# Kernel tuning notes

Measured on AMD Instinct MI355X. Metric: run time of the kernel, lower is better.

Reference implementation:

```python
import jax, jax.numpy as jnp
import numpy as np

EMB = 64
N_LEFT = 50000
N_RIGHT = 50000
N_EDGES = 1000000
EPS = 1e-5


def _block(x, w1, b1, w2, b2):
    # Linear -> BatchNorm1d(batch stats, no affine) -> (Dropout=id, eval) -> Linear -> ReLU
    h = x @ w1 + b1
    mu = h.mean(axis=0)
    var = h.var(axis=0)  # biased, matches torch BN normalization
    h = (h - mu) / jnp.sqrt(var + EPS)
    return jax.nn.relu(h @ w2 + b2)


def _lin_init(key, fan_in, fan_out):
    k1, k2 = jax.random.split(key)
    bound = 1.0 / np.sqrt(fan_in)
    w = jax.random.uniform(k1, (fan_in, fan_out), minval=-bound, maxval=bound, dtype=jnp.float32)
    b = jax.random.uniform(k2, (fan_out,), minval=-bound, maxval=bound, dtype=jnp.float32)
    return w, b


def setup_inputs() -> dict:
    key = jax.random.key(0)
    ks = jax.random.split(key, 16)
    inp = {}
    inp['left_features'] = jax.random.normal(ks[0], (N_LEFT, EMB), dtype=jnp.float32)
    inp['right_features'] = jax.random.normal(ks[1], (N_RIGHT, EMB), dtype=jnp.float32)
    inp['edge_features'] = jax.random.normal(ks[2], (N_EDGES, EMB), dtype=jnp.float32)
    src = jax.random.randint(ks[3], (N_EDGES,), 0, N_LEFT, dtype=jnp.int32)
    dst = jax.random.randint(ks[4], (N_EDGES,), 0, N_RIGHT, dtype=jnp.int32)
    inp['edge_index'] = jnp.stack([src, dst], axis=0)
    # feature_module_right (applied to both i and j, as in the original message())
    inp['fmr_w1'], inp['fmr_b1'] = _lin_init(ks[5], EMB, EMB)
    inp['fmr_w2'], inp['fmr_b2'] = _lin_init(ks[6], EMB, EMB)
    # feature_module_edge
    inp['fme_w1'], inp['fme_b1'] = _lin_init(ks[7], EMB, EMB)
    inp['fme_w2'], inp['fme_b2'] = _lin_init(ks[8], EMB, EMB)
    # feature_module_final (3*emb -> emb -> emb)
    inp['fmf_w1'], inp['fmf_b1'] = _lin_init(ks[9], 3 * EMB, EMB)
    inp['fmf_w2'], inp['fmf_b2'] = _lin_init(ks[10], EMB, EMB)
    # output_module (2*emb -> emb -> emb)
    inp['out_w1'], inp['out_b1'] = _lin_init(ks[11], 2 * EMB, EMB)
    inp['out_w2'], inp['out_b2'] = _lin_init(ks[12], EMB, EMB)
    return inp


def reference(left_features, right_features, edge_features, edge_index,
              fmr_w1, fmr_b1, fmr_w2, fmr_b2,
              fme_w1, fme_b1, fme_w2, fme_b2,
              fmf_w1, fmf_b1, fmf_w2, fmf_b2,
              out_w1, out_b1, out_w2, out_b2):
    src = edge_index[0]  # index into left (source / j)
    dst = edge_index[1]  # index into right (target / i)

    x_i = right_features[dst]           # [E, emb] gathered targets
    x_j = left_features[src]            # [E, emb] gathered sources

    m_i = _block(x_i, fmr_w1, fmr_b1, fmr_w2, fmr_b2)
    m_e = _block(edge_features, fme_w1, fme_b1, fme_w2, fme_b2)
    m_j = _block(x_j, fmr_w1, fmr_b1, fmr_w2, fmr_b2)  # feature_module_right reused, as in source

    msg = _block(jnp.concatenate([m_i, m_e, m_j], axis=1),
                 fmf_w1, fmf_b1, fmf_w2, fmf_b2)        # [E, emb]

    # mean aggregation over target nodes
    agg = jax.ops.segment_sum(msg, dst, num_segments=N_RIGHT)
    cnt = jax.ops.segment_sum(jnp.ones((msg.shape[0],), msg.dtype), dst, num_segments=N_RIGHT)
    agg = agg / jnp.maximum(cnt, 1.0)[:, None]

    out = _block(jnp.concatenate([agg, right_features], axis=1),
                 out_w1, out_b1, out_w2, out_b2)        # [N_right, emb]
    return out
```

## Files before the change

### kernel.cpp

```cpp
#include <hip/hip_runtime.h>

#define EMB 64
#define BNEPS 1e-5f
#define NSLAB 8
#define NSLABH 32
#define MAXSLOT 128
#define MAXOVF 65536

typedef unsigned short u16;
typedef float f32x4 __attribute__((ext_vector_type(4)));
typedef short bf16x8 __attribute__((ext_vector_type(8)));
typedef short bf16x4 __attribute__((ext_vector_type(4)));

__device__ __forceinline__ float bf2f(u16 u){
  union { unsigned int i; float f; } v; v.i = ((unsigned int)u) << 16; return v.f;
}
__device__ __forceinline__ u16 f2bf(float x){
  union { float f; unsigned int i; } v; v.f = x;
  unsigned int r = v.i + 0x7FFFu + ((v.i >> 16) & 1u);
  return (u16)(r >> 16);
}
__device__ __forceinline__ void atomAddF(float* p, float v){
  __hip_atomic_fetch_add(p, v, __ATOMIC_RELAXED, __HIP_MEMORY_SCOPE_AGENT);
}

__global__ void kzero(float* __restrict__ fz, long nf){
  long i0 = (long)blockIdx.x * blockDim.x + threadIdx.x;
  long st = (long)gridDim.x * blockDim.x;
  for (long i = i0; i < nf; i += st) fz[i] = 0.f;
}

__global__ void kcount(const int* __restrict__ src, const int* __restrict__ dst,
                       int E, int* __restrict__ cs, int* __restrict__ cd,
                       int* __restrict__ sort1, int* __restrict__ ovfCnt,
                       int* __restrict__ ovfList){
  int e = blockIdx.x * blockDim.x + threadIdx.x;
  int st = gridDim.x * blockDim.x;
  for (; e < E; e += st){
    atomicAdd(&cs[src[e]], 1);
    int d = dst[e];
    int i = atomicAdd(&cd[d], 1);
    if (sort1){
      if (i < MAXSLOT){
        sort1[(size_t)d * MAXSLOT + i] = e;
      } else {
        int oi = atomicAdd(ovfCnt, 1);
        if (oi < MAXOVF) ovfList[oi] = e;
      }
    }
  }
}

__global__ __launch_bounds__(1024) void ktiles(const int* __restrict__ cd, int NR,
                       int* __restrict__ tcnt, int* __restrict__ tlist){
  __shared__ int wsum[16];
  __shared__ int wbase[16];
  __shared__ int bbase;
  int tid = threadIdx.x, lane = tid & 63, w = tid >> 6;
  int d = blockIdx.x * 1024 + tid;
  int nt = 0, c = 0;
  if (d < NR){
    c = cd[d];
    if (c > 0){
      nt = (c + 15) >> 4;
      if (nt > (MAXSLOT / 16)) nt = MAXSLOT / 16;
    }
  }
  int inc = nt;
  #pragma unroll
  for (int m = 1; m < 64; m <<= 1){
    int v = __shfl_up(inc, m);
    if (lane >= m) inc += v;
  }
  if (lane == 63) wsum[w] = inc;
  __syncthreads();
  if (tid == 0){
    int acc = 0;
    #pragma unroll
    for (int k = 0; k < 16; k++){ wbase[k] = acc; acc += wsum[k]; }
    bbase = acc ? atomicAdd(tcnt, acc) : 0;
  }
  __syncthreads();
  int my = bbase + wbase[w] + inc - nt;
  for (int t = 0; t < nt; t++){
    int vc = c - t * 16; if (vc > 16) vc = 16;
    tlist[my + t] = (vc << 20) | (d << 3) | t;
  }
}

__global__ __launch_bounds__(256) void kgram(const float* __restrict__ X,
    const int* __restrict__ cnt, int N,
    float* __restrict__ mupart, float* __restrict__ Spart){
  __shared__ float xs[16][EMB];
  __shared__ float cs[16];
  int t = threadIdx.x;
  int a = t >> 2, bb = (t & 3) << 4;
  int row = t >> 4, k0 = (t & 15) << 2;
  float g[16];
  #pragma unroll
  for (int i = 0; i < 16; i++) g[i] = 0.f;
  float mup = 0.f;
  int base0 = blockIdx.x * 16, stride = gridDim.x * 16;
  f32x4 xreg = {0.f,0.f,0.f,0.f};
  float creg = 0.f;
  {
    int n = base0 + row;
    if (n < N) xreg = *(const f32x4*)(X + (size_t)n * EMB + k0);
    if (t < 16){
      int n2 = base0 + t;
      creg = (n2 < N) ? (float)cnt[n2] : 0.f;
    }
  }
  for (int n0 = base0; n0 < N; n0 += stride){
    *(f32x4*)&xs[row][k0] = xreg;
    if (t < 16) cs[t] = creg;
    __syncthreads();
    int n1 = n0 + stride;
    if (n1 < N){
      int n = n1 + row;
      xreg = (n < N) ? *(const f32x4*)(X + (size_t)n * EMB + k0) : (f32x4){0.f,0.f,0.f,0.f};
      if (t < 16){
        int n2 = n1 + t;
        creg = (n2 < N) ? (float)cnt[n2] : 0.f;
      }
    }
    #pragma unroll
    for (int rr = 0; rr < 16; rr++){
      float xa = cs[rr] * xs[rr][a];
      const float4* x4 = (const float4*)&xs[rr][bb];
      #pragma unroll
      for (int i4 = 0; i4 < 4; i4++){
        float4 v = x4[i4];
        g[4*i4+0] += xa * v.x; g[4*i4+1] += xa * v.y;
        g[4*i4+2] += xa * v.z; g[4*i4+3] += xa * v.w;
      }
    }
    if (t < EMB){
      #pragma unroll
      for (int rr = 0; rr < 16; rr++) mup += cs[rr] * xs[rr][t];
    }
    __syncthreads();
  }
  float* Sp = Spart + (size_t)blockIdx.x * 4096;
  #pragma unroll
  for (int i4 = 0; i4 < 4; i4++)
    *(f32x4*)&Sp[a * EMB + bb + i4 * 4] = *(f32x4*)&g[i4 * 4];
  if (t < EMB) mupart[(size_t)blockIdx.x * 64 + t] = mup;
}

struct GredArgs { const float *Sp, *mp; int nb; float *So, *mo; };
__global__ __launch_bounds__(256) void kgreduce3(GredArgs g0, GredArgs g1, GredArgs g2){
  int job = blockIdx.x >> 4, sub = blockIdx.x & 15;
  GredArgs G = (job == 0) ? g0 : (job == 1) ? g1 : g2;
  int e = sub * 256 + threadIdx.x;
  float s0 = 0.f, s1 = 0.f, s2 = 0.f, s3 = 0.f;
  int b = 0;
  for (; b + 3 < G.nb; b += 4){
    s0 += G.Sp[(size_t)(b    ) * 4096 + e];
    s1 += G.Sp[(size_t)(b + 1) * 4096 + e];
    s2 += G.Sp[(size_t)(b + 2) * 4096 + e];
    s3 += G.Sp[(size_t)(b + 3) * 4096 + e];
  }
  for (; b < G.nb; b++) s0 += G.Sp[(size_t)b * 4096 + e];
  G.So[e] = (s0 + s1) + (s2 + s3);
  if (sub == 0 && threadIdx.x < 64){
    float m0 = 0.f, m1 = 0.f, m2 = 0.f, m3 = 0.f;
    int c = 0;
    for (; c + 3 < G.nb; c += 4){
      m0 += G.mp[(size_t)(c    ) * 64 + threadIdx.x];
      m1 += G.mp[(size_t)(c + 1) * 64 + threadIdx.x];
      m2 += G.mp[(size_t)(c + 2) * 64 + threadIdx.x];
      m3 += G.mp[(size_t)(c + 3) * 64 + threadIdx.x];
    }
    for (; c < G.nb; c++) m0 += G.mp[(size_t)c * 64 + threadIdx.x];
    G.mo[threadIdx.x] = (m0 + m1) + (m2 + m3);
  }
}

__global__ __launch_bounds__(256) void kprepm(const float* __restrict__ XE, int N,
    float* __restrict__ mupart, float* __restrict__ Spart, u16* __restrict__ XEb){
  __shared__ __align__(16) u16 XT[64 * 72];
  int t = threadIdx.x, l = t & 63, wv = t >> 6, g = l >> 4, e16 = l & 15;
  f32x4 C[4];
  #pragma unroll
  for (int mb = 0; mb < 4; mb++) C[mb] = (f32x4){0.f,0.f,0.f,0.f};
  float ms[4] = {0.f, 0.f, 0.f, 0.f};
  int ntiles = N >> 6;
  int T = blockIdx.x;
  f32x4 vr0 = {0,0,0,0}, vr1 = {0,0,0,0}, vr2 = {0,0,0,0}, vr3 = {0,0,0,0};
  if (T < ntiles){
    #pragma unroll
    for (int i = 0; i < 4; i++){
      int c = t + i * 256;
      int row = c >> 4, k0 = (c & 15) << 2;
      f32x4 v = *(const f32x4*)(XE + ((size_t)T * 64 + row) * EMB + k0);
      if (i == 0) vr0 = v; else if (i == 1) vr1 = v; else if (i == 2) vr2 = v; else vr3 = v;
    }
  }
  for (; T < ntiles; T += gridDim.x){
    #pragma unroll
    for (int i = 0; i < 4; i++){
      int c = t + i * 256;
      int row = c >> 4, k0 = (c & 15) << 2;
      f32x4 v = (i == 0) ? vr0 : (i == 1) ? vr1 : (i == 2) ? vr2 : vr3;
      u16 w4[4];
      #pragma unroll
      for (int q = 0; q < 4; q++){
        ms[q] += v[q];
        w4[q] = f2bf(v[q]);
        XT[(k0 + q) * 72 + row] = w4[q];
      }
      if (XEb) *(bf16x4*)(XEb + ((size_t)T * 64 + row) * EMB + k0) = *(bf16x4*)w4;
    }
    __syncthreads();
    int T2 = T + gridDim.x;
    if (T2 < ntiles){
      #pragma unroll
      for (int i = 0; i < 4; i++){
        int c = t + i * 256;
        int row = c >> 4, k0 = (c & 15) << 2;
        f32x4 v = *(const f32x4*)(XE + ((size_t)T2 * 64 + row) * EMB + k0);
        if (i == 0) vr0 = v; else if (i == 1) vr1 = v; else if (i == 2) vr2 = v; else vr3 = v;
      }
    }
    #pragma unroll
    for (int kf = 0; kf < 2; kf++){
      bf16x8 fr[4];
      #pragma unroll
      for (int mb = 0; mb < 4; mb++)
        fr[mb] = *(const bf16x8*)&XT[(mb*16 + e16) * 72 + kf*32 + g*8];
      bf16x8 bfr = *(const bf16x8*)&XT[(wv*16 + e16) * 72 + kf*32 + g*8];
      #pragma unroll
      for (int mb = 0; mb < 4; mb++)
        C[mb] = __builtin_amdgcn_mfma_f32_16x16x32_bf16(fr[mb], bfr, C[mb], 0, 0, 0);
    }
    __syncthreads();
  }
  float* Sp = Spart + (size_t)blockIdx.x * 4096;
  #pragma unroll
  for (int mb = 0; mb < 4; mb++)
    #pragma unroll
    for (int r = 0; r < 4; r++)
      Sp[(mb*16 + g*4 + r) * EMB + wv*16 + e16] = C[mb][r];
  __syncthreads();
  float* red = (float*)XT;
  #pragma unroll
  for (int q = 0; q < 4; q++){
    float x = ms[q];
    x += __shfl_xor(x, 16); x += __shfl_xor(x, 32);
    if (l < 16) red[(wv*16 + l)*4 + q] = x;
  }
  __syncthreads();
  if (t < 64){
    int k = t >> 2, q = t & 3;
    float s = red[(k)*4+q] + red[(16+k)*4+q] + red[(32+k)*4+q] + red[(48+k)*4+q];
    mupart[(size_t)blockIdx.x * 64 + k*4 + q] = s;
  }
}

struct EffwArgs {
  const float *mu, *S, *w1, *b1, *w2, *b2;
  float *We, *be;
};
__global__ __launch_bounds__(256) void keffw3(EffwArgs a0, EffwArgs a1, EffwArgs a2,
    float invN, u16* __restrict__ fragA1, u16* __restrict__ fragA2,
    const float* __restrict__ fA2src){
  EffwArgs A = (blockIdx.x == 0) ? a0 : (blockIdx.x == 1) ? a1 : a2;
  const float *musum = A.mu, *S = A.S, *w1 = A.w1, *b1 = A.b1, *w2 = A.w2, *b2 = A.b2;
  float *Weff = A.We, *beff = A.be;
  __shared__ float mu[EMB];
  __shared__ float C[EMB][EMB];
  __shared__ float W1p[EMB][EMB + 1];
  __shared__ float c1[EMB];
  __shared__ float istd[EMB];
  __shared__ float red[256];
  int t = threadIdx.x;
  if (t < EMB) mu[t] = musum[t] * invN;
  __syncthreads();
  for (int e = t; e < EMB * EMB; e += 256){
    int k = e >> 6, l = e & 63;
    C[k][l] = S[e] * invN - mu[k] * mu[l];
  }
  __syncthreads();
  {
    int j = t & 63, kg = t >> 6;
    float part = 0.f;
    for (int k = kg * 16; k < kg * 16 + 16; k++){
      float inner = 0.f;
      for (int l = 0; l < EMB; l++) inner += C[k][l] * w1[l * EMB + j];
      part += w1[k * EMB + j] * inner;
    }
    red[t] = part;
  }
  __syncthreads();
  if (t < EMB){
    float var = red[t] + red[t + 64] + red[t + 128] + red[t + 192];
    float is = 1.0f / sqrtf(var + BNEPS);
    istd[t] = is;
    float muh = 0.f;
    for (int k = 0; k < EMB; k++) muh += mu[k] * w1[k * EMB + t];
    muh += b1[t];
    c1[t] = (b1[t] - muh) * is;
  }
  __syncthreads();
  for (int e = t; e < EMB * EMB; e += 256){
    int k = e >> 6, j = e & 63;
    W1p[k][j] = w1[e] * istd[j];
  }
  __syncthreads();
  {
    int k = t >> 2, j2b = (t & 3) << 4;
    float acc[16];
    #pragma unroll
    for (int i = 0; i < 16; i++) acc[i] = 0.f;
    for (int j = 0; j < EMB; j++){
      float wp = W1p[k][j];
      const float* w2r = &w2[j * EMB + j2b];
      #pragma unroll
      for (int i = 0; i < 16; i++) acc[i] += wp * w2r[i];
    }
    #pragma unroll
    for (int i = 0; i < 16; i++){
      Weff[k * EMB + j2b + i] = acc[i];
      C[k][j2b + i] = acc[i];
    }
  }
  if (t < EMB){
    float acc = b2[t];
    for (int j = 0; j < EMB; j++) acc += c1[j] * w2[j * EMB + t];
    beff[t] = acc;
  }
  __syncthreads();
  if (blockIdx.x == 2){
    for (int ent = t; ent < 512; ent += 256){
      int mb = ent >> 7, kf = (ent >> 6) & 1, l = ent & 63;
      int g = l >> 4, e16 = l & 15;
      u16 out[8];
      #pragma unroll
      for (int i = 0; i < 8; i++)
        out[i] = f2bf(C[kf*32 + g*8 + i][mb*16 + e16]);
      *(bf16x8*)(fragA1 + ent * 8) = *(bf16x8*)out;
    }
  } else if (blockIdx.x == 1){
    for (int ent = t; ent < 512; ent += 256){
      int mb = ent >> 7, kf = (ent >> 6) & 1, l = ent & 63;
      int g = l >> 4, e16 = l & 15;
      u16 out[8];
      #pragma unroll
      for (int i = 0; i < 8; i++){
        int row = (kf + 2*(i>>2))*16 + g*4 + (i&3);
        out[i] = f2bf(fA2src[row * EMB + mb*16 + e16]);
      }
      *(bf16x8*)(fragA2 + ent * 8) = *(bf16x8*)out;
    }
  }
}

__global__ __launch_bounds__(256) void knodeMP(const float* __restrict__ X,
    const float* __restrict__ Weff, const float* __restrict__ beff,
    const float* __restrict__ Wslice, int N, u16* __restrict__ P){
  __shared__ float xs[4][EMB];
  __shared__ float ms[4][EMB];
  __shared__ float be[EMB];
  int t = threadIdx.x, r = t >> 6, j = t & 63;
  float wA[EMB], wB[EMB];
  #pragma unroll
  for (int k = 0; k < EMB; k++){ wA[k] = Weff[k * EMB + j]; wB[k] = Wslice[k * EMB + j]; }
  if (t < EMB) be[t] = beff[t];
  __syncthreads();
  for (int n0 = blockIdx.x * 4; n0 < N; n0 += gridDim.x * 4){
    int n = n0 + r; bool ok = n < N;
    xs[r][j] = ok ? X[(size_t)n * EMB + j] : 0.f;
    __syncthreads();
    float a0 = be[j], a1 = 0.f, a2 = 0.f, a3 = 0.f;
    const float4* x4 = (const float4*)xs[r];
    #pragma unroll
    for (int kb = 0; kb < 16; kb++){
      float4 v = x4[kb];
      a0 += v.x * wA[4*kb]; a1 += v.y * wA[4*kb+1];
      a2 += v.z * wA[4*kb+2]; a3 += v.w * wA[4*kb+3];
    }
    ms[r][j] = fmaxf((a0 + a1) + (a2 + a3), 0.f);
    __syncthreads();
    float p0 = 0.f, p1 = 0.f, p2 = 0.f, p3 = 0.f;
    const float4* m4 = (const float4*)ms[r];
    #pragma unroll
    for (int kb = 0; kb < 16; kb++){
      float4 v = m4[kb];
      p0 += v.x * wB[4*kb]; p1 += v.y * wB[4*kb+1];
      p2 += v.z * wB[4*kb+2]; p3 += v.w * wB[4*kb+3];
    }
    if (ok) P[(size_t)n * EMB + j] = f2bf((p0 + p1) + (p2 + p3));
    __syncthreads();
  }
}

__global__ __launch_bounds__(256) void kpass1m(const float* __restrict__ XE,
    const u16* __restrict__ XEb,
    const int* __restrict__ srcv, const int* __restrict__ dstv,
    const u16* __restrict__ fragA1, const u16* __restrict__ fragA2,
    const float* __restrict__ beff_e, const float* __restrict__ bf1,
    const u16* __restrict__ Pib, const u16* __restrict__ Pjb, int ntiles,
    u16* __restrict__ hbf, float* __restrict__ hsum, float* __restrict__ hsq){
  __shared__ float cs[256];
  int t = threadIdx.x, l = t & 63, wv = t >> 6, g = l >> 4, e16 = l & 15;
  cs[t] = 0.f;
  bf16x8 a1w[4][2], a2w[4][2];
  #pragma unroll
  for (int mb = 0; mb < 4; mb++)
    #pragma unroll
    for (int kf = 0; kf < 2; kf++){
      a1w[mb][kf] = *(const bf16x8*)(fragA1 + ((size_t)((mb*2+kf)*64 + l)) * 8);
      a2w[mb][kf] = *(const bf16x8*)(fragA2 + ((size_t)((mb*2+kf)*64 + l)) * 8);
    }
  f32x4 b1v[4], b2v[4];
  #pragma unroll
  for (int mb = 0; mb < 4; mb++)
    #pragma unroll
    for (int r = 0; r < 4; r++){
      b1v[mb][r] = beff_e[mb*16 + g*4 + r];
      b2v[mb][r] = bf1[mb*16 + g*4 + r];
    }
  f32x4 ps[4], pq[4];
  #pragma unroll
  for (int mb = 0; mb < 4; mb++){ ps[mb] = (f32x4){0,0,0,0}; pq[mb] = (f32x4){0,0,0,0}; }

  int gw = blockIdx.x * 4 + wv, nw = gridDim.x * 4;
  int d_n = 0, s_n = 0;
  if (gw < ntiles){ d_n = dstv[gw*16 + e16]; s_n = srcv[gw*16 + e16]; }
  for (int T = gw; T < ntiles; T += nw){
    int d = d_n, s = s_n;
    bf16x8 xf0, xf1;
    if (XEb){
      const u16* xr = XEb + (size_t)(T*16 + e16) * EMB;
      xf0 = *(const bf16x8*)(xr + g*8);
      xf1 = *(const bf16x8*)(xr + 32 + g*8);
    } else {
      const float* xr = XE + (size_t)(T*16 + e16) * EMB;
      f32x4 x0 = *(const f32x4*)(xr + g*8);
      f32x4 x1 = *(const f32x4*)(xr + g*8 + 4);
      f32x4 x2 = *(const f32x4*)(xr + 32 + g*8);
      f32x4 x3 = *(const f32x4*)(xr + 36 + g*8);
      #pragma unroll
      for (int q = 0; q < 4; q++){
        xf0[q]   = (short)f2bf(x0[q]); xf0[4+q] = (short)f2bf(x1[q]);
        xf1[q]   = (short)f2bf(x2[q]); xf1[4+q] = (short)f2bf(x3[q]);
      }
    }
    const u16* pib = Pib + (size_t)d * EMB;
    const u16* pjb = Pjb + (size_t)s * EMB;
    bf16x4 piv[4], pjv[4];
    #pragma unroll
    for (int mb = 0; mb < 4; mb++){
      piv[mb] = *(const bf16x4*)(pib + mb*16 + g*4);
      pjv[mb] = *(const bf16x4*)(pjb + mb*16 + g*4);
    }
    int T2 = T + nw;
    if (T2 < ntiles){ d_n = dstv[T2*16 + e16]; s_n = srcv[T2*16 + e16]; }
    f32x4 C2[4];
    #pragma unroll
    for (int mb = 0; mb < 4; mb++)
      #pragma unroll
      for (int r = 0; r < 4; r++)
        C2[mb][r] = b2v[mb][r] + bf2f((u16)piv[mb][r]) + bf2f((u16)pjv[mb][r]);
    f32x4 C1[4];
    #pragma unroll
    for (int mb = 0; mb < 4; mb++) C1[mb] = b1v[mb];
    #pragma unroll
    for (int mb = 0; mb < 4; mb++){
      C1[mb] = __builtin_amdgcn_mfma_f32_16x16x32_bf16(a1w[mb][0], xf0, C1[mb], 0, 0, 0);
      C1[mb] = __builtin_amdgcn_mfma_f32_16x16x32_bf16(a1w[mb][1], xf1, C1[mb], 0, 0, 0);
    }
    bf16x8 mfr0, mfr1;
    #pragma unroll
    for (int q = 0; q < 4; q++){
      mfr0[q]   = (short)f2bf(fmaxf(C1[0][q], 0.f));
      mfr0[4+q] = (short)f2bf(fmaxf(C1[2][q], 0.f));
      mfr1[q]   = (short)f2bf(fmaxf(C1[1][q], 0.f));
      mfr1[4+q] = (short)f2bf(fmaxf(C1[3][q], 0.f));
    }
    #pragma unroll
    for (int mb = 0; mb < 4; mb++){
      C2[mb] = __builtin_amdgcn_mfma_f32_16x16x32_bf16(a2w[mb][0], mfr0, C2[mb], 0, 0, 0);
      C2[mb] = __builtin_amdgcn_mfma_f32_16x16x32_bf16(a2w[mb][1], mfr1, C2[mb], 0, 0, 0);
    }
    #pragma unroll
    for (int mb = 0; mb < 4; mb++){ ps[mb] += C2[mb]; pq[mb] += C2[mb] * C2[mb]; }
    u16* hr = hbf + (size_t)(T*16 + e16) * EMB;
    #pragma unroll
    for (int mb = 0; mb < 4; mb++){
      u16 hv[4];
      #pragma unroll
      for (int q = 0; q < 4; q++) hv[q] = f2bf(C2[mb][q]);
      *(bf16x4*)(hr + mb*16 + g*4) = *(bf16x4*)hv;
    }
  }
  __syncthreads();
  #pragma unroll
  for (int mb = 0; mb < 4; mb++)
    #pragma unroll
    for (int r = 0; r < 4; r++){
      float v = ps[mb][r], u = pq[mb][r];
      #pragma unroll
      for (int m = 1; m < 16; m <<= 1){ v += __shfl_xor(v, m); u += __shfl_xor(u, m); }
      if (e16 == 0){
        int col = mb*16 + g*4 + r;
        atomicAdd(&cs[col], v);
        atomicAdd(&cs[128 + col], u);
      }
    }
  __syncthreads();
  int slab = blockIdx.x & (NSLABH - 1);
  if (t < 64) atomAddF(&hsum[slab * 64 + t], cs[t]);
  else if (t < 128) atomAddF(&hsq[slab * 64 + t - 64], cs[128 + t - 64]);
}

__global__ __launch_bounds__(256) void kbnfold(const float* __restrict__ hsum,
    const float* __restrict__ hsq, int nslab, float invN, const float* __restrict__ w2,
    const float* __restrict__ b2, float* __restrict__ W2p, float* __restrict__ b2p,
    u16* __restrict__ F){
  __shared__ float mu[EMB], istd[EMB];
  int t = threadIdx.x;
  if (t < EMB){
    float m = 0.f, q = 0.f;
    for (int s = 0; s < nslab; s++){ m += hsum[s * 64 + t]; q += hsq[s * 64 + t]; }
    m *= invN;
    float var = q * invN - m * m;
    mu[t] = m; istd[t] = 1.0f / sqrtf(var + BNEPS);
  }
  __syncthreads();
  for (int e = t; e < EMB * EMB; e += 256){
    int k = e >> 6;
    W2p[e] = istd[k] * w2[e];
  }
  if (t < EMB){
    float acc = b2[t];
    for (int k = 0; k < EMB; k++) acc -= mu[k] * istd[k] * w2[k * EMB + t];
    b2p[t] = acc;
  }
  if (F){
    for (int ent = t; ent < 512; ent += 256){
      int mb = ent >> 7, kf = (ent >> 6) & 1, l = ent & 63;
      int g = (l >> 4), e16 = l & 15;
      u16 out[8];
      #pragma unroll
      for (int i = 0; i < 8; i++){
        int row = kf*32 + g*8 + i;
        out[i] = f2bf(istd[row] * w2[row * EMB + mb*16 + e16]);
      }
      *(bf16x8*)(F + ent * 8) = *(bf16x8*)out;
    }
  }
}

__global__ __launch_bounds__(256) void kpass2s(const u16* __restrict__ hb,
    const int* __restrict__ sort1, const int* __restrict__ tcnt,
    const int* __restrict__ tlist, const u16* __restrict__ fragW2,
    const float* __restrict__ b2p, float* __restrict__ agg){
  int t = threadIdx.x, l = t & 63, wv = t >> 6, g = l >> 4, e16 = l & 15;
  bf16x8 w2f[4][2];
  #pragma unroll
  for (int nb = 0; nb < 4; nb++)
    #pragma unroll
    for (int kf = 0; kf < 2; kf++)
      w2f[nb][kf] = *(const bf16x8*)(fragW2 + ((size_t)((nb*2+kf)*64 + l)) * 8);
  float bv[4];
  #pragma unroll
  for (int nb = 0; nb < 4; nb++) bv[nb] = b2p[nb*16 + e16];

  int tc = *tcnt;
  int gw = blockIdx.x * 4 + wv, nw = gridDim.x * 4;
  if (gw >= tc) return;
  int w_n = tlist[gw];
  int se_n = sort1[(size_t)((w_n >> 3) & 0x1FFFF) * MAXSLOT + (w_n & 7) * 16 + e16];
  for (int m = gw; m < tc; m += nw){
    int w = w_n, se = se_n;
    int m2 = m + nw;
    if (m2 < tc) w_n = tlist[m2];
    int d = (w >> 3) & 0x1FFFF, vc = w >> 20;
    int eid = (e16 < vc) ? se : 0;
    const u16* hr = hb + (size_t)eid * EMB;
    bf16x8 a0 = *(const bf16x8*)(hr + g*8);
    bf16x8 a1 = *(const bf16x8*)(hr + 32 + g*8);
    if (m2 < tc)
      se_n = sort1[(size_t)((w_n >> 3) & 0x1FFFF) * MAXSLOT + (w_n & 7) * 16 + e16];
    f32x4 C[4];
    #pragma unroll
    for (int nb = 0; nb < 4; nb++) C[nb] = (f32x4){0.f,0.f,0.f,0.f};
    #pragma unroll
    for (int nb = 0; nb < 4; nb++){
      C[nb] = __builtin_amdgcn_mfma_f32_16x16x32_bf16(a0, w2f[nb][0], C[nb], 0, 0, 0);
      C[nb] = __builtin_amdgcn_mfma_f32_16x16x32_bf16(a1, w2f[nb][1], C[nb], 0, 0, 0);
    }
    int r0 = g * 4;
    #pragma unroll
    for (int nb = 0; nb < 4; nb++){
      float s = 0.f;
      if (r0 + 0 < vc) s += fmaxf(C[nb][0] + bv[nb], 0.f);
      if (r0 + 1 < vc) s += fmaxf(C[nb][1] + bv[nb], 0.f);
      if (r0 + 2 < vc) s += fmaxf(C[nb][2] + bv[nb], 0.f);
      if (r0 + 3 < vc) s += fmaxf(C[nb][3] + bv[nb], 0.f);
      s += __shfl_xor(s, 16);
      s += __shfl_xor(s, 32);
      if (g == 0) atomAddF(&agg[(size_t)d * EMB + nb*16 + e16], s);
    }
  }
}

__global__ __launch_bounds__(256) void kpass2d(const u16* __restrict__ hb,
    const int* __restrict__ dstv, const u16* __restrict__ fragW2,
    const float* __restrict__ b2p, int ntiles, float* __restrict__ agg){
  int t = threadIdx.x, l = t & 63, wv = t >> 6, g = l >> 4, e16 = l & 15;
  bf16x8 w2f[4][2];
  #pragma unroll
  for (int nb = 0; nb < 4; nb++)
    #pragma unroll
    for (int kf = 0; kf < 2; kf++)
      w2f[nb][kf] = *(const bf16x8*)(fragW2 + ((size_t)((nb*2+kf)*64 + l)) * 8);
  float bv[4];
  #pragma unroll
  for (int nb = 0; nb < 4; nb++) bv[nb] = b2p[nb*16 + e16];
  int gw = blockIdx.x * 4 + wv, nw = gridDim.x * 4;
  for (int T = gw; T < ntiles; T += nw){
    const u16* hr = hb + (size_t)(T*16 + e16) * EMB;
    bf16x8 a0 = *(const bf16x8*)(hr + g*8);
    bf16x8 a1 = *(const bf16x8*)(hr + 32 + g*8);
    int4 dd = *(const int4*)(dstv + T*16 + g*4);
    f32x4 C[4];
    #pragma unroll
    for (int nb = 0; nb < 4; nb++) C[nb] = (f32x4){0.f,0.f,0.f,0.f};
    #pragma unroll
    for (int nb = 0; nb < 4; nb++){
      C[nb] = __builtin_amdgcn_mfma_f32_16x16x32_bf16(a0, w2f[nb][0], C[nb], 0, 0, 0);
      C[nb] = __builtin_amdgcn_mfma_f32_16x16x32_bf16(a1, w2f[nb][1], C[nb], 0, 0, 0);
    }
    int dr[4] = {dd.x, dd.y, dd.z, dd.w};
    #pragma unroll
    for (int r = 0; r < 4; r++){
      float* ap = agg + (size_t)dr[r] * EMB + e16;
      #pragma unroll
      for (int nb = 0; nb < 4; nb++)
        atomAddF(ap + nb*16, fmaxf(C[nb][r] + bv[nb], 0.f));
    }
  }
}

__global__ void kpass2f(const u16* __restrict__ hb, const int* __restrict__ ovfList,
    const int* __restrict__ ovfCnt, const int* __restrict__ dstv,
    const float* __restrict__ W2p, const float* __restrict__ b2p, float* __restrict__ agg){
  int cnt = *ovfCnt;
  if (cnt > MAXOVF) cnt = MAXOVF;
  for (int c = blockIdx.x * blockDim.x + threadIdx.x; c < cnt * 64;
       c += gridDim.x * blockDim.x){
    int e = ovfList[c >> 6], j = c & 63;
    const u16* hr = hb + (size_t)e * EMB;
    float acc = b2p[j];
    for (int k = 0; k < 64; k++) acc += bf2f(hr[k]) * W2p[k * EMB + j];
    atomAddF(&agg[(size_t)dstv[e] * EMB + j], fmaxf(acc, 0.f));
  }
}

__global__ __launch_bounds__(256) void kout1(const float* __restrict__ agg,
    const int* __restrict__ cnt, const float* __restrict__ right,
    const float* __restrict__ ow1, const float* __restrict__ ob1, int N,
    float* __restrict__ h_o, float* __restrict__ osum, float* __restrict__ osq){
  __shared__ float xs[4][2 * EMB];
  __shared__ float bsh[EMB];
  __shared__ float red[256];
  int t = threadIdx.x, r = t >> 6, j = t & 63;
  float wc[2 * EMB];
  #pragma unroll
  for (int k = 0; k < 2 * EMB; k++) wc[k] = ow1[k * EMB + j];
  if (t < EMB) bsh[t] = ob1[t];
  __syncthreads();
  float psum = 0.f, psq = 0.f;
  for (int n0 = blockIdx.x * 4; n0 < N; n0 += gridDim.x * 4){
    int n = n0 + r; bool ok = n < N;
    if (ok){
      float c = fmaxf((float)cnt[n], 1.f);
      xs[r][j] = agg[(size_t)n * EMB + j] / c;
      xs[r][EMB + j] = right[(size_t)n * EMB + j];
    } else { xs[r][j] = 0.f; xs[r][EMB + j] = 0.f; }
    __syncthreads();
    float a0 = bsh[j], a1 = 0.f, a2 = 0.f, a3 = 0.f;
    const float4* x4 = (const float4*)xs[r];
    #pragma unroll
    for (int kb = 0; kb < 32; kb++){
      float4 v = x4[kb];
      a0 += v.x * wc[4*kb]; a1 += v.y * wc[4*kb+1];
      a2 += v.z * wc[4*kb+2]; a3 += v.w * wc[4*kb+3];
    }
    if (ok){
      float h = (a0 + a1) + (a2 + a3);
      h_o[(size_t)n * EMB + j] = h;
      psum += h; psq += h * h;
    }
    __syncthreads();
  }
  int slab = blockIdx.x & (NSLAB - 1);
  red[t] = psum; __syncthreads();
  if (t < EMB) atomAddF(&osum[slab * 64 + t], red[t] + red[t + 64] + red[t + 128] + red[t + 192]);
  __syncthreads();
  red[t] = psq; __syncthreads();
  if (t < EMB) atomAddF(&osq[slab * 64 + t], red[t] + red[t + 64] + red[t + 128] + red[t + 192]);
}

__global__ __launch_bounds__(256) void kout2(const float* __restrict__ h_o,
    const float* __restrict__ W2o, const float* __restrict__ b2o, int N,
    float* __restrict__ out){
  __shared__ float hs[4][EMB];
  __shared__ float bsh[EMB];
  int t = threadIdx.x, r = t >> 6, j = t & 63;
  float wc[EMB];
  #pragma unroll
  for (int k = 0; k < EMB; k++) wc[k] = W2o[k * EMB + j];
  if (t < EMB) bsh[t] = b2o[t];
  __syncthreads();
  for (int n0 = blockIdx.x * 4; n0 < N; n0 += gridDim.x * 4){
    int n = n0 + r; bool ok = n < N;
    hs[r][j] = ok ? h_o[(size_t)n * EMB + j] : 0.f;
    __syncthreads();
    float a0 = bsh[j], a1 = 0.f, a2 = 0.f, a3 = 0.f;
    const float4* h4 = (const float4*)hs[r];
    #pragma unroll
    for (int kb = 0; kb < 16; kb++){
      float4 v = h4[kb];
      a0 += v.x * wc[4*kb]; a1 += v.y * wc[4*kb+1];
      a2 += v.z * wc[4*kb+2]; a3 += v.w * wc[4*kb+3];
    }
    if (ok) out[(size_t)n * EMB + j] = fmaxf((a0 + a1) + (a2 + a3), 0.f);
    __syncthreads();
  }
}

extern "C" void kernel_launch(void* const* d_in, const int* in_sizes, int n_in,
                              void* d_out, int out_size, void* d_ws, size_t ws_size,
                              hipStream_t stream){
  const float* left   = (const float*)d_in[0];
  const float* right  = (const float*)d_in[1];
  const float* edgef  = (const float*)d_in[2];
  const int*   eidx   = (const int*)d_in[3];
  const float* fmr_w1 = (const float*)d_in[4];  const float* fmr_b1 = (const float*)d_in[5];
  const float* fmr_w2 = (const float*)d_in[6];  const float* fmr_b2 = (const float*)d_in[7];
  const float* fme_w1 = (const float*)d_in[8];  const float* fme_b1 = (const float*)d_in[9];
  const float* fme_w2 = (const float*)d_in[10]; const float* fme_b2 = (const float*)d_in[11];
  const float* fmf_w1 = (const float*)d_in[12]; const float* fmf_b1 = (const float*)d_in[13];
  const float* fmf_w2 = (const float*)d_in[14]; const float* fmf_b2 = (const float*)d_in[15];
  const float* ow1    = (const float*)d_in[16]; const float* ob1    = (const float*)d_in[17];
  const float* ow2    = (const float*)d_in[18]; const float* ob2    = (const float*)d_in[19];

  int NL = in_sizes[0] / EMB;
  int NR = in_sizes[1] / EMB;
  int E  = in_sizes[2] / EMB;
  const int* srcv = eidx;
  const int* dstv = eidx + E;

  char* base = (char*)d_ws;
  size_t o = 0;
  u16* hbf = (u16*)(base + o);      o += (size_t)E * EMB * sizeof(u16);
  u16* P_i  = (u16*)(base + o); o += (size_t)NR * EMB * sizeof(u16);
  u16* P_j  = (u16*)(base + o); o += (size_t)NL * EMB * sizeof(u16);
  float* h_o  = (float*)(base + o); o += (size_t)NR * EMB * 4;
  float* Weff_i = (float*)(base + o); o += EMB * EMB * 4;
  float* beff_i = (float*)(base + o); o += EMB * 4;
  float* Weff_j = (float*)(base + o); o += EMB * EMB * 4;
  float* beff_j = (float*)(base + o); o += EMB * 4;
  float* Weff_e = (float*)(base + o); o += EMB * EMB * 4;
  float* beff_e = (float*)(base + o); o += EMB * 4;
  float* W2p  = (float*)(base + o); o += EMB * EMB * 4;
  float* b2p  = (float*)(base + o); o += EMB * 4;
  float* W2o  = (float*)(base + o); o += EMB * EMB * 4;
  float* b2o  = (float*)(base + o); o += EMB * 4;
  u16* fragA1 = (u16*)(base + o); o += 512 * 8 * sizeof(u16);
  u16* fragA2 = (u16*)(base + o); o += 512 * 8 * sizeof(u16);
  u16* fragW2 = (u16*)(base + o); o += 512 * 8 * sizeof(u16);
  int* ovfList = (int*)(base + o); o += MAXOVF * sizeof(int);
  int* tlist   = (int*)(base + o); o += (size_t)NR * (MAXSLOT / 16) * sizeof(int);
  char* zstart = base + o;
  float* agg     = (float*)(base + o); o += (size_t)NR * EMB * 4;
  int* cnt_dst   = (int*)(base + o);   o += (size_t)NR * 4;
  int* cnt_src   = (int*)(base + o);   o += (size_t)NL * 4;
  int* ovfCnt    = (int*)(base + o);   o += 64;
  int* tileCnt   = (int*)(base + o);   o += 64;
  float* musum_i = (float*)(base + o); o += NSLAB * EMB * 4;
  float* S_i     = (float*)(base + o); o += NSLAB * EMB * EMB * 4;
  float* musum_j = (float*)(base + o); o += NSLAB * EMB * 4;
  float* S_j     = (float*)(base + o); o += NSLAB * EMB * EMB * 4;
  float* musum_e = (float*)(base + o); o += NSLAB * EMB * 4;
  float* S_e     = (float*)(base + o); o += NSLAB * EMB * EMB * 4;
  float* hsum    = (float*)(base + o); o += NSLABH * EMB * 4;
  float* hsq     = (float*)(base + o); o += NSLABH * EMB * 4;
  float* osum    = (float*)(base + o); o += NSLAB * EMB * 4;
  float* osq     = (float*)(base + o); o += NSLAB * EMB * 4;
  long zn = (long)(((base + o) - zstart) / 4);
  int* sort1 = nullptr;
  {
    size_t s1b = (size_t)NR * MAXSLOT * sizeof(int);
    if (o + s1b <= ws_size){ sort1 = (int*)(base + o); o += s1b; }
  }
  u16* XEb = nullptr;
  {
    size_t xeb_bytes = (size_t)E * EMB * sizeof(u16);
    if (o + xeb_bytes <= ws_size){ XEb = (u16*)(base + o); o += xeb_bytes; }
  }

  const int NBG = 512;
  const int NBE = 1024;
  float* Spart_i  = (float*)hbf;
  float* Spart_j  = Spart_i + (size_t)NBG * 4096;
  float* Spart_e  = Spart_j + (size_t)NBG * 4096;
  float* mupart_i = Spart_e + (size_t)NBE * 4096;
  float* mupart_j = mupart_i + (size_t)NBG * 64;
  float* mupart_e = mupart_j + (size_t)NBG * 64;

  float invE = 1.0f / (float)E;
  float invNR = 1.0f / (float)NR;
  int ntE = E >> 4;

  kzero<<<1024, 256, 0, stream>>>((float*)zstart, zn);
  kcount<<<512, 256, 0, stream>>>(srcv, dstv, E, cnt_src, cnt_dst, sort1, ovfCnt, ovfList);
  if (sort1) ktiles<<<(NR + 1023) / 1024, 1024, 0, stream>>>(cnt_dst, NR, tileCnt, tlist);
  kprepm<<<NBE, 256, 0, stream>>>(edgef, E, mupart_e, Spart_e, XEb);
  kgram<<<NBG, 256, 0, stream>>>(right, cnt_dst, NR, mupart_i, Spart_i);
  kgram<<<NBG, 256, 0, stream>>>(left,  cnt_src, NL, mupart_j, Spart_j);
  {
    GredArgs g0 = {Spart_i, mupart_i, NBG, S_i, musum_i};
    GredArgs g1 = {Spart_j, mupart_j, NBG, S_j, musum_j};
    GredArgs g2 = {Spart_e, mupart_e, NBE, S_e, musum_e};
    kgreduce3<<<48, 256, 0, stream>>>(g0, g1, g2);
  }
  {
    EffwArgs a0 = {musum_i, S_i, fmr_w1, fmr_b1, fmr_w2, fmr_b2, Weff_i, beff_i};
    EffwArgs a1 = {musum_j, S_j, fmr_w1, fmr_b1, fmr_w2, fmr_b2, Weff_j, beff_j};
    EffwArgs a2 = {musum_e, S_e, fme_w1, fme_b1, fme_w2, fme_b2, Weff_e, beff_e};
    keffw3<<<3, 256, 0, stream>>>(a0, a1, a2, invE, fragA1, fragA2, fmf_w1 + EMB * EMB);
  }
  knodeMP<<<1024, 256, 0, stream>>>(right, Weff_i, beff_i, fmf_w1,                 NR, P_i);
  knodeMP<<<1024, 256, 0, stream>>>(left,  Weff_j, beff_j, fmf_w1 + 2 * EMB * EMB, NL, P_j);
  kpass1m<<<1536, 256, 0, stream>>>(edgef, XEb, srcv, dstv, fragA1, fragA2, beff_e,
                                    fmf_b1, P_i, P_j, ntE, hbf, hsum, hsq);
  kbnfold<<<1, 256, 0, stream>>>(hsum, hsq, NSLABH, invE, fmf_w2, fmf_b2, W2p, b2p, fragW2);
  if (sort1){
    kpass2s<<<2048, 256, 0, stream>>>(hbf, sort1, tileCnt, tlist, fragW2, b2p, agg);
    kpass2f<<<16, 256, 0, stream>>>(hbf, ovfList, ovfCnt, dstv, W2p, b2p, agg);
  } else {
    kpass2d<<<2048, 256, 0, stream>>>(hbf, dstv, fragW2, b2p, ntE, agg);
  }
  kout1<<<1024, 256, 0, stream>>>(agg, cnt_dst, right, ow1, ob1, NR, h_o, osum, osq);
  kbnfold<<<1, 256, 0, stream>>>(osum, osq, NSLAB, invNR, ow2, ob2, W2o, b2o, (u16*)nullptr);
  kout2<<<1024, 256, 0, stream>>>(h_o, W2o, b2o, NR, (float*)d_out);
}
```

Baseline: 730.3 us.

## Permute node projections for contiguous gathers, fold output BN into kout2

knodeMP now writes each projected node row in a permuted order that matches the MFMA accumulator layout. kpass1m can then fetch each lane's 16 values of the gathered P_i/P_j rows with two 16-byte loads per row, where it previously issued four 8-byte loads per row. The final BN fold kernel is removed and its work is done redundantly in every kout2 block, saving one launch at the cost of each block reading ow2 and the stats. kpass1m's grid also grows from 1536 to 2048 blocks.

Result: faster. 710.7 us (-2.7%).

```diff
diff --git a/kernel.cpp b/kernel.cpp
--- a/kernel.cpp
+++ b/kernel.cpp
@@ -363,6 +363,7 @@
   __shared__ float ms[4][EMB];
   __shared__ float be[EMB];
   int t = threadIdx.x, r = t >> 6, j = t & 63;
+  int pos = ((j >> 2) & 3) * 16 + (j >> 4) * 4 + (j & 3);
   float wA[EMB], wB[EMB];
   #pragma unroll
   for (int k = 0; k < EMB; k++){ wA[k] = Weff[k * EMB + j]; wB[k] = Wslice[k * EMB + j]; }
@@ -390,7 +391,7 @@
       p0 += v.x * wB[4*kb]; p1 += v.y * wB[4*kb+1];
       p2 += v.z * wB[4*kb+2]; p3 += v.w * wB[4*kb+3];
     }
-    if (ok) P[(size_t)n * EMB + j] = f2bf((p0 + p1) + (p2 + p3));
+    if (ok) P[(size_t)n * EMB + pos] = f2bf((p0 + p1) + (p2 + p3));
     __syncthreads();
   }
 }
@@ -447,22 +448,23 @@
         xf1[q]   = (short)f2bf(x2[q]); xf1[4+q] = (short)f2bf(x3[q]);
       }
     }
-    const u16* pib = Pib + (size_t)d * EMB;
-    const u16* pjb = Pjb + (size_t)s * EMB;
-    bf16x4 piv[4], pjv[4];
-    #pragma unroll
-    for (int mb = 0; mb < 4; mb++){
-      piv[mb] = *(const bf16x4*)(pib + mb*16 + g*4);
-      pjv[mb] = *(const bf16x4*)(pjb + mb*16 + g*4);
-    }
+    const u16* pib = Pib + (size_t)d * EMB + g*16;
+    const u16* pjb = Pjb + (size_t)s * EMB + g*16;
+    bf16x8 pi0 = *(const bf16x8*)(pib);
+    bf16x8 pi1 = *(const bf16x8*)(pib + 8);
+    bf16x8 pj0 = *(const bf16x8*)(pjb);
+    bf16x8 pj1 = *(const bf16x8*)(pjb + 8);
     int T2 = T + nw;
     if (T2 < ntiles){ d_n = dstv[T2*16 + e16]; s_n = srcv[T2*16 + e16]; }
     f32x4 C2[4];
     #pragma unroll
     for (int mb = 0; mb < 4; mb++)
       #pragma unroll
-      for (int r = 0; r < 4; r++)
-        C2[mb][r] = b2v[mb][r] + bf2f((u16)piv[mb][r]) + bf2f((u16)pjv[mb][r]);
+      for (int r = 0; r < 4; r++){
+        float pv = bf2f((u16)((mb < 2) ? pi0[(mb&1)*4 + r] : pi1[(mb&1)*4 + r]));
+        float qv = bf2f((u16)((mb < 2) ? pj0[(mb&1)*4 + r] : pj1[(mb&1)*4 + r]));
+        C2[mb][r] = b2v[mb][r] + pv + qv;
+      }
     f32x4 C1[4];
     #pragma unroll
     for (int mb = 0; mb < 4; mb++) C1[mb] = b1v[mb];
@@ -706,15 +708,30 @@
 }
 
 __global__ __launch_bounds__(256) void kout2(const float* __restrict__ h_o,
-    const float* __restrict__ W2o, const float* __restrict__ b2o, int N,
+    const float* __restrict__ osum, const float* __restrict__ osq, float invN,
+    const float* __restrict__ ow2, const float* __restrict__ ob2, int N,
     float* __restrict__ out){
   __shared__ float hs[4][EMB];
   __shared__ float bsh[EMB];
+  __shared__ float istd[EMB], mus[EMB];
   int t = threadIdx.x, r = t >> 6, j = t & 63;
+  if (t < EMB){
+    float m = 0.f, q = 0.f;
+    #pragma unroll
+    for (int s = 0; s < NSLAB; s++){ m += osum[s * 64 + t]; q += osq[s * 64 + t]; }
+    m *= invN;
+    float var = q * invN - m * m;
+    mus[t] = m; istd[t] = 1.0f / sqrtf(var + BNEPS);
+  }
+  __syncthreads();
+  if (t < EMB){
+    float acc = ob2[t];
+    for (int k = 0; k < EMB; k++) acc -= mus[k] * istd[k] * ow2[k * EMB + t];
+    bsh[t] = acc;
+  }
   float wc[EMB];
   #pragma unroll
-  for (int k = 0; k < EMB; k++) wc[k] = W2o[k * EMB + j];
-  if (t < EMB) bsh[t] = b2o[t];
+  for (int k = 0; k < EMB; k++) wc[k] = istd[k] * ow2[k * EMB + j];
   __syncthreads();
   for (int n0 = blockIdx.x * 4; n0 < N; n0 += gridDim.x * 4){
     int n = n0 + r; bool ok = n < N;
@@ -769,8 +786,6 @@
   float* beff_e = (float*)(base + o); o += EMB * 4;
   float* W2p  = (float*)(base + o); o += EMB * EMB * 4;
   float* b2p  = (float*)(base + o); o += EMB * 4;
-  float* W2o  = (float*)(base + o); o += EMB * EMB * 4;
-  float* b2o  = (float*)(base + o); o += EMB * 4;
   u16* fragA1 = (u16*)(base + o); o += 512 * 8 * sizeof(u16);
   u16* fragA2 = (u16*)(base + o); o += 512 * 8 * sizeof(u16);
   u16* fragW2 = (u16*)(base + o); o += 512 * 8 * sizeof(u16);
@@ -837,7 +852,7 @@
   }
   knodeMP<<<1024, 256, 0, stream>>>(right, Weff_i, beff_i, fmf_w1,                 NR, P_i);
   knodeMP<<<1024, 256, 0, stream>>>(left,  Weff_j, beff_j, fmf_w1 + 2 * EMB * EMB, NL, P_j);
-  kpass1m<<<1536, 256, 0, stream>>>(edgef, XEb, srcv, dstv, fragA1, fragA2, beff_e,
+  kpass1m<<<2048, 256, 0, stream>>>(edgef, XEb, srcv, dstv, fragA1, fragA2, beff_e,
                                     fmf_b1, P_i, P_j, ntE, hbf, hsum, hsq);
   kbnfold<<<1, 256, 0, stream>>>(hsum, hsq, NSLABH, invE, fmf_w2, fmf_b2, W2p, b2p, fragW2);
   if (sort1){
@@ -847,6 +862,5 @@
     kpass2d<<<2048, 256, 0, stream>>>(hbf, dstv, fragW2, b2p, ntE, agg);
   }
   kout1<<<1024, 256, 0, stream>>>(agg, cnt_dst, right, ow1, ob1, NR, h_o, osum, osq);
-  kbnfold<<<1, 256, 0, stream>>>(osum, osq, NSLAB, invNR, ow2, ob2, W2o, b2o, (u16*)nullptr);
-  kout2<<<1024, 256, 0, stream>>>(h_o, W2o, b2o, NR, (float*)d_out);
-}
+  kout2<<<1024, 256, 0, stream>>>(h_o, osum, osq, invNR, ow2, ob2, NR, (float*)d_out);
+}
```
